# Kernel tuning notes

Hardware: AMD Instinct MI355X
Metric: run time of the kernel (lower is better)

Reference implementation:

```python
import jax, jax.numpy as jnp
import numpy as np

C = 16       # celltypes
N = 20000    # nodes per PPI graph
D = 192      # in_channels == out_channels*heads (residual constraint)
H = 3        # node_heads
CO = 64      # out_channels per head
E = 320000   # edges per PPI graph
T = 32       # tissue nodes
K = 8        # neighbors per tissue
M = C + T    # metagraph nodes
R = 4        # metagraph relations
EM = 256     # edges per metagraph relation
S = 128      # sem_att_channels
TU = 100     # tissue_update iterations


def setup_inputs():
    key = jax.random.key(0)
    k = jax.random.split(key, 16)
    g = lambda kk, shp, sc: jax.random.normal(kk, shp, jnp.float32) * sc
    return {
        "ppi_x": g(k[0], (C, N, D), 1.0),
        "metagraph_x": g(k[1], (M, D), 1.0),
        "ppi_lin": g(k[2], (C, D, H * CO), 0.07),
        "ppi_att_src": g(k[3], (C, H, CO), 0.1),
        "ppi_att_dst": g(k[4], (C, H, CO), 0.1),
        "ppi_bias": jnp.zeros((C, H * CO), jnp.float32),
        "meta_lin": g(k[5], (R, H * CO, H * CO), 0.07),
        "meta_att_src": g(k[6], (R, H, CO), 0.1),
        "meta_att_dst": g(k[7], (R, H, CO), 0.1),
        "meta_bias": jnp.zeros((R, H * CO), jnp.float32),
        "W_sem": g(k[8], (H * CO, S), 0.08),
        "b_sem": jnp.zeros((S,), jnp.float32),
        "q_sem": g(k[9], (S,), 0.1),
        "ppi_edges": jax.random.randint(k[10], (C, 2, E), 0, N, dtype=jnp.int32),
        "meta_edges": jax.random.randint(k[11], (R, 2, EM), 0, M, dtype=jnp.int32),
        "tissue_nb": jax.random.randint(k[12], (T, K), 0, M, dtype=jnp.int32),
    }


def gat(x, lin, att_s, att_d, bias, edge, n):
    """PyG-style GATConv, concat heads. x:[n,Din], edge:[2,E] (src,dst)."""
    h = (x @ lin).reshape(n, H, CO)
    a_s = (h * att_s).sum(-1)   # [n,H]
    a_d = (h * att_d).sum(-1)
    src, dst = edge[0], edge[1]
    e = jax.nn.leaky_relu(a_s[src] + a_d[dst], negative_slope=0.2)  # [E,H]
    emax = jax.lax.stop_gradient(jax.ops.segment_max(e, dst, num_segments=n))
    emax = jnp.where(jnp.isfinite(emax), emax, 0.0)
    ex = jnp.exp(e - emax[dst])
    denom = jax.ops.segment_sum(ex, dst, num_segments=n)          # [n,H]
    out = jax.ops.segment_sum(ex[:, :, None] * h[src], dst, num_segments=n)
    out = out / jnp.where(denom > 0.0, denom, 1.0)[:, :, None]
    return out.reshape(n, H * CO) + bias


def sem_attention(out, W, b, q):
    """Semantic attention over relations. out:[M,R,Dh]."""
    w = jnp.tanh(jnp.einsum('mrd,ds->mrs', out, W) + b)
    beta = jax.nn.softmax(jnp.einsum('mrs,s->mr', w, q), axis=1)
    return jnp.einsum('mrd,mr->md', out, beta)


def forward(ppi_x, metagraph_x, ppi_lin, ppi_att_src, ppi_att_dst, ppi_bias,
            meta_lin, meta_att_src, meta_att_dst, meta_bias,
            W_sem, b_sem, q_sem, ppi_edges, meta_edges, tissue_nb):
    mx = metagraph_x
    # residual GAT per celltype, mean-pooled into the metagraph celltype row
    for c in range(C):
        att = ppi_x[c] + gat(ppi_x[c], ppi_lin[c], ppi_att_src[c], ppi_att_dst[c],
                             ppi_bias[c], ppi_edges[c], N)
        mx = mx.at[c].add(att.mean(0))
    # sequential (Gauss-Seidel) tissue-neighbor mean diffusion, TU sweeps
    def step(m, t):
        return m.at[C + t].set(m[tissue_nb[t]].mean(0)), None
    def sweep(m, _):
        m, _ = jax.lax.scan(step, m, jnp.arange(T))
        return m, None
    mx, _ = jax.lax.scan(sweep, mx, None, length=TU)
    # multi-relation metagraph GAT + semantic attention fusion
    outs = jnp.stack([gat(mx, meta_lin[r], meta_att_src[r], meta_att_dst[r],
                          meta_bias[r], meta_edges[r], M) for r in range(R)], axis=1)
    outs = jax.nn.relu(outs)  # torch applies relu after stacking
    return sem_attention(outs, W_sem, b_sem, q_sem)


def reference(ppi_x, metagraph_x, ppi_lin, ppi_att_src, ppi_att_dst, ppi_bias,
              meta_lin, meta_att_src, meta_att_dst, meta_bias,
              W_sem, b_sem, q_sem, ppi_edges, meta_edges, tissue_nb):
    return forward(ppi_x, metagraph_x, ppi_lin, ppi_att_src, ppi_att_dst, ppi_bias,
                   meta_lin, meta_att_src, meta_att_dst, meta_bias,
                   W_sem, b_sem, q_sem, ppi_edges, meta_edges, tissue_nb)
```

## Files before the change

### kernel.cpp

```cpp
#include <hip/hip_runtime.h>

#define CT 16
#define NN 20000
#define EE 320000
#define MM 48
#define RR 4
#define EMM 256
#define NRANGE 64
#define NPR 313
#define CAP 5632
#define MAGIC 13721941ULL

#define OFF_MEANX 0
#define OFF_P     3072
#define OFF_CNTD  12288
#define OFF_CNTS  13312
#define ZERO_FLOATS 14336
#define OFF_COMB  14336
#define OFF_AS    2574336
#define OFF_AD    3854336
#define OFF_U     5134336
#define OFF_V     5143552
#define OFF_MX    5152768
#define OFF_HH    5161984
#define OFF_OUTS  5198848
#define OFF_BIND  5235712
#define OFF_BINS  11002880

__device__ inline unsigned bucket_of(int d) {
    return (unsigned)(((unsigned long long)(unsigned)d * MAGIC) >> 32);
}

__global__ __launch_bounds__(192) void k_prep(const float* __restrict__ lin,
        const float* __restrict__ as_g, const float* __restrict__ ad_g,
        float* __restrict__ U, float* __restrict__ V) {
    int c = blockIdx.x, d = threadIdx.x;
    const float* L  = lin + ((size_t)c * 192 + d) * 192;
    const float* As = as_g + c * 192;
    const float* Ad = ad_g + c * 192;
#pragma unroll
    for (int h = 0; h < 3; ++h) {
        float u = 0.f, v = 0.f;
        for (int j = 0; j < 64; ++j) {
            float lv = L[h * 64 + j];
            u += lv * As[h * 64 + j];
            v += lv * Ad[h * 64 + j];
        }
        U[c * 576 + h * 192 + d] = u;
        V[c * 576 + h * 192 + d] = v;
    }
}

__global__ __launch_bounds__(256) void k_front(const int* __restrict__ edges,
        int* __restrict__ cntD, int* __restrict__ cntS,
        int* __restrict__ binD, int* __restrict__ binS,
        const float* __restrict__ x, const float* __restrict__ U,
        const float* __restrict__ V, float* __restrict__ a_s,
        float* __restrict__ a_d, float* __restrict__ meanx) {
    __shared__ __align__(16) float smem[3456];
    int tid = threadIdx.x;
    if (blockIdx.x < 1024) {
        int wg = blockIdx.x;
        int ct = (wg & 7) * 2 + ((wg >> 3) & 1);
        int part = wg >> 4;
        int wave = tid >> 6;
        int* histD = (int*)smem;
        int* histS = histD + 256;
        int* curD  = histS + 256;
        int* curS  = curD + 64;
        if (tid < NRANGE) {
            histD[0 * 64 + tid] = 0; histD[1 * 64 + tid] = 0;
            histD[2 * 64 + tid] = 0; histD[3 * 64 + tid] = 0;
            histS[0 * 64 + tid] = 0; histS[1 * 64 + tid] = 0;
            histS[2 * 64 + tid] = 0; histS[3 * 64 + tid] = 0;
        }
        __syncthreads();
        const int* srcp = edges + (size_t)ct * 2 * EE;
        const int* dstp = srcp + EE;
        const int4* s4 = (const int4*)srcp;
        const int4* d4 = (const int4*)dstp;
        int base4 = part * 1250;
        for (int i = tid; i < 1250; i += 256) {
            int4 dv = d4[base4 + i];
            int4 sv = s4[base4 + i];
            atomicAdd(&histD[wave * 64 + bucket_of(dv.x)], 1);
            atomicAdd(&histD[wave * 64 + bucket_of(dv.y)], 1);
            atomicAdd(&histD[wave * 64 + bucket_of(dv.z)], 1);
            atomicAdd(&histD[wave * 64 + bucket_of(dv.w)], 1);
            atomicAdd(&histS[wave * 64 + bucket_of(sv.x)], 1);
            atomicAdd(&histS[wave * 64 + bucket_of(sv.y)], 1);
            atomicAdd(&histS[wave * 64 + bucket_of(sv.z)], 1);
            atomicAdd(&histS[wave * 64 + bucket_of(sv.w)], 1);
        }
        __syncthreads();
        if (tid < NRANGE) {
            int t = histD[tid] + histD[64 + tid] + histD[128 + tid] + histD[192 + tid];
            curD[tid] = atomicAdd(&cntD[ct * NRANGE + tid], t);
            int t2 = histS[tid] + histS[64 + tid] + histS[128 + tid] + histS[192 + tid];
            curS[tid] = atomicAdd(&cntS[ct * NRANGE + tid], t2);
        }
        __syncthreads();
        int* bD = binD + (size_t)ct * NRANGE * CAP;
        int* bS = binS + (size_t)ct * NRANGE * CAP;
#define EMIT2(ss, dd) { int pk = ((ss) << 15) | (dd); \
        unsigned bd = bucket_of(dd); int so = atomicAdd(&curD[bd], 1); \
        if (so < CAP) bD[bd * CAP + so] = pk; \
        unsigned bs = bucket_of(ss); int s2 = atomicAdd(&curS[bs], 1); \
        if (s2 < CAP) bS[bs * CAP + s2] = pk; }
        for (int i = tid; i < 1250; i += 256) {
            int4 dv = d4[base4 + i];
            int4 sv = s4[base4 + i];
            EMIT2(sv.x, dv.x); EMIT2(sv.y, dv.y); EMIT2(sv.z, dv.z); EMIT2(sv.w, dv.w);
        }
#undef EMIT2
    } else {
        int idx = blockIdx.x - 1024;
        int c = idx & 15;
        int start = (idx >> 4) * 160;
        int lane = tid & 63;
        int wave = tid >> 6;
        float* A = smem;
        float* blk = smem + 3264;
        if (tid < 192) blk[tid] = 0.f;
        float u0[3], u1[3], u2[3], v0[3], v1[3], v2[3];
#pragma unroll
        for (int h = 0; h < 3; ++h) {
            u0[h] = U[c * 576 + h * 192 + lane];
            u1[h] = U[c * 576 + h * 192 + 64 + lane];
            u2[h] = U[c * 576 + h * 192 + 128 + lane];
            v0[h] = V[c * 576 + h * 192 + lane];
            v1[h] = V[c * 576 + h * 192 + 64 + lane];
            v2[h] = V[c * 576 + h * 192 + 128 + lane];
        }
        __syncthreads();
        const float* xc = x + (size_t)c * NN * 192;
        float* asn = a_s + (size_t)c * NN * 4;
        float* adn = a_d + (size_t)c * NN * 4;
        float m0 = 0.f, m1 = 0.f, m2 = 0.f;
        float* Aa = A + (wave * 2) * 408;
        float* Ab = A + (wave * 2 + 1) * 408;
        int rrow = lane >> 3, seg = lane & 7;
        for (int i = 0; i < 20; ++i) {
            int na = start + wave + 8 * i;
            int nb = na + 4;
            const float* xa = xc + (size_t)na * 192;
            const float* xb = xc + (size_t)nb * 192;
            float xa0 = xa[lane], xa1 = xa[64 + lane], xa2 = xa[128 + lane];
            float xb0 = xb[lane], xb1 = xb[64 + lane], xb2 = xb[128 + lane];
            m0 += xa0 + xb0; m1 += xa1 + xb1; m2 += xa2 + xb2;
            Aa[0 * 68 + lane] = xa0 * u0[0] + xa1 * u1[0] + xa2 * u2[0];
            Aa[1 * 68 + lane] = xa0 * u0[1] + xa1 * u1[1] + xa2 * u2[1];
            Aa[2 * 68 + lane] = xa0 * u0[2] + xa1 * u1[2] + xa2 * u2[2];
            Aa[3 * 68 + lane] = xa0 * v0[0] + xa1 * v1[0] + xa2 * v2[0];
            Aa[4 * 68 + lane] = xa0 * v0[1] + xa1 * v1[1] + xa2 * v2[1];
            Aa[5 * 68 + lane] = xa0 * v0[2] + xa1 * v1[2] + xa2 * v2[2];
            Ab[0 * 68 + lane] = xb0 * u0[0] + xb1 * u1[0] + xb2 * u2[0];
            Ab[1 * 68 + lane] = xb0 * u0[1] + xb1 * u1[1] + xb2 * u2[1];
            Ab[2 * 68 + lane] = xb0 * u0[2] + xb1 * u1[2] + xb2 * u2[2];
            Ab[3 * 68 + lane] = xb0 * v0[0] + xb1 * v1[0] + xb2 * v2[0];
            Ab[4 * 68 + lane] = xb0 * v0[1] + xb1 * v1[1] + xb2 * v2[1];
            Ab[5 * 68 + lane] = xb0 * v0[2] + xb1 * v1[2] + xb2 * v2[2];
            float sa = 0.f, sb = 0.f;
            if (lane < 48) {
                const float4* pa = (const float4*)(Aa + rrow * 68 + seg * 8);
                const float4* pb = (const float4*)(Ab + rrow * 68 + seg * 8);
                float4 a0 = pa[0], a1 = pa[1];
                float4 b0 = pb[0], b1 = pb[1];
                sa = ((a0.x + a0.y) + (a0.z + a0.w)) + ((a1.x + a1.y) + (a1.z + a1.w));
                sb = ((b0.x + b0.y) + (b0.z + b0.w)) + ((b1.x + b1.y) + (b1.z + b1.w));
            }
            sa += __shfl_xor(sa, 1, 64); sb += __shfl_xor(sb, 1, 64);
            sa += __shfl_xor(sa, 2, 64); sb += __shfl_xor(sb, 2, 64);
            sa += __shfl_xor(sa, 4, 64); sb += __shfl_xor(sb, 4, 64);
            if (lane < 48 && seg == 0) {
                if (rrow < 3) { asn[na * 4 + rrow] = sa;     asn[nb * 4 + rrow] = sb; }
                else          { adn[na * 4 + rrow - 3] = sa; adn[nb * 4 + rrow - 3] = sb; }
            }
        }
        atomicAdd(&blk[lane], m0);
        atomicAdd(&blk[64 + lane], m1);
        atomicAdd(&blk[128 + lane], m2);
        __syncthreads();
        if (tid < 192) atomicAdd(&meanx[c * 192 + tid], blk[tid]);
    }
}

__device__ inline void map_ct(int wg, int& ct, int& j) {
    int xcd = wg & 7;
    ct = xcd * 2 + ((wg >> 3) & 1);
    j = wg >> 4;
}

__global__ __launch_bounds__(512) void k_eden_b(const int* __restrict__ bin,
        const int* __restrict__ cnt, const float* __restrict__ a_s,
        const float* __restrict__ a_d, float* __restrict__ comb) {
    int ct, bkt;
    map_ct(blockIdx.x, ct, bkt);
    int lo = bkt * NPR;
    int nnode = NN - lo < NPR ? NN - lo : NPR;
    int tid = threadIdx.x;
    __shared__ float adl[NPR * 3];
    __shared__ float den[NPR * 3];
    const float4* as4 = (const float4*)(a_s + (size_t)ct * NN * 4);
    const float4* ad4 = (const float4*)(a_d + (size_t)ct * NN * 4);
    for (int m = tid; m < nnode; m += 512) {
        float4 v = ad4[lo + m];
        adl[m * 3] = v.x; adl[m * 3 + 1] = v.y; adl[m * 3 + 2] = v.z;
    }
    for (int o = tid; o < nnode * 3; o += 512) den[o] = 0.f;
    __syncthreads();
    int n = cnt[ct * NRANGE + bkt]; if (n > CAP) n = CAP;
    const int* bc = bin + ((size_t)ct * NRANGE + bkt) * CAP;
    for (int i = tid; i < n; i += 512) {
        int v = bc[i];
        int d = v & 32767, s = v >> 15;
        int dl = d - lo;
        float4 av = as4[s];
        float e0 = av.x + adl[dl * 3];     e0 = e0 >= 0.f ? e0 : 0.2f * e0;
        float e1 = av.y + adl[dl * 3 + 1]; e1 = e1 >= 0.f ? e1 : 0.2f * e1;
        float e2 = av.z + adl[dl * 3 + 2]; e2 = e2 >= 0.f ? e2 : 0.2f * e2;
        atomicAdd(&den[dl * 3],     __expf(e0));
        atomicAdd(&den[dl * 3 + 1], __expf(e1));
        atomicAdd(&den[dl * 3 + 2], __expf(e2));
    }
    __syncthreads();
    float4* cb = (float4*)(comb + (size_t)ct * NN * 8);
    for (int m = tid; m < nnode; m += 512) {
        float d0 = den[m * 3], d1 = den[m * 3 + 1], d2 = den[m * 3 + 2];
        float4 a, b;
        a.x = adl[m * 3]; a.y = adl[m * 3 + 1]; a.z = adl[m * 3 + 2]; a.w = 0.f;
        b.x = d0 > 0.f ? 1.f / d0 : 0.f;
        b.y = d1 > 0.f ? 1.f / d1 : 0.f;
        b.z = d2 > 0.f ? 1.f / d2 : 0.f;
        b.w = 0.f;
        cb[(size_t)(lo + m) * 2]     = a;
        cb[(size_t)(lo + m) * 2 + 1] = b;
    }
}

__global__ __launch_bounds__(512) void k_es_p(const int* __restrict__ bin,
        const int* __restrict__ cnt, const float* __restrict__ a_s,
        const float* __restrict__ comb, const float* __restrict__ x,
        float* __restrict__ p) {
    int ct, bkt;
    map_ct(blockIdx.x, ct, bkt);
    int lo = bkt * NPR;
    int nnode = NN - lo < NPR ? NN - lo : NPR;
    int tid = threadIdx.x;
    __shared__ float asl[NPR * 3];
    __shared__ float sl[NPR * 3];
    __shared__ float blk[576];
    const float4* as4 = (const float4*)(a_s + (size_t)ct * NN * 4);
    const float4* cb  = (const float4*)(comb + (size_t)ct * NN * 8);
    for (int m = tid; m < nnode; m += 512) {
        float4 v = as4[lo + m];
        asl[m * 3] = v.x; asl[m * 3 + 1] = v.y; asl[m * 3 + 2] = v.z;
    }
    for (int o = tid; o < nnode * 3; o += 512) sl[o] = 0.f;
    for (int o = tid; o < 576; o += 512) blk[o] = 0.f;
    __syncthreads();
    int n = cnt[ct * NRANGE + bkt]; if (n > CAP) n = CAP;
    const int* bc = bin + ((size_t)ct * NRANGE + bkt) * CAP;
    for (int i = tid; i < n; i += 512) {
        int v = bc[i];
        int d = v & 32767, s = v >> 15;
        int slc = s - lo;
        float4 av = cb[(size_t)d * 2];
        float4 dv = cb[(size_t)d * 2 + 1];
        float e0 = asl[slc * 3]     + av.x; e0 = e0 >= 0.f ? e0 : 0.2f * e0;
        float e1 = asl[slc * 3 + 1] + av.y; e1 = e1 >= 0.f ? e1 : 0.2f * e1;
        float e2 = asl[slc * 3 + 2] + av.z; e2 = e2 >= 0.f ? e2 : 0.2f * e2;
        atomicAdd(&sl[slc * 3],     __expf(e0) * dv.x);
        atomicAdd(&sl[slc * 3 + 1], __expf(e1) * dv.y);
        atomicAdd(&sl[slc * 3 + 2], __expf(e2) * dv.z);
    }
    __syncthreads();
    int lane = tid & 63;
    int wave = tid >> 6;
    const float* xc = x + (size_t)ct * NN * 192;
    float a00 = 0, a01 = 0, a02 = 0, a10 = 0, a11 = 0, a12 = 0, a20 = 0, a21 = 0, a22 = 0;
    for (int m = wave; m < nnode; m += 8) {
        float s0 = sl[m * 3], s1 = sl[m * 3 + 1], s2 = sl[m * 3 + 2];
        const float* xr = xc + (size_t)(lo + m) * 192;
        float x0 = xr[lane], x1 = xr[64 + lane], x2 = xr[128 + lane];
        a00 += s0 * x0; a01 += s0 * x1; a02 += s0 * x2;
        a10 += s1 * x0; a11 += s1 * x1; a12 += s1 * x2;
        a20 += s2 * x0; a21 += s2 * x1; a22 += s2 * x2;
    }
    atomicAdd(&blk[0 * 192 + lane], a00);
    atomicAdd(&blk[0 * 192 + 64 + lane], a01);
    atomicAdd(&blk[0 * 192 + 128 + lane], a02);
    atomicAdd(&blk[1 * 192 + lane], a10);
    atomicAdd(&blk[1 * 192 + 64 + lane], a11);
    atomicAdd(&blk[1 * 192 + 128 + lane], a12);
    atomicAdd(&blk[2 * 192 + lane], a20);
    atomicAdd(&blk[2 * 192 + 64 + lane], a21);
    atomicAdd(&blk[2 * 192 + 128 + lane], a22);
    __syncthreads();
    for (int o = tid; o < 576; o += 512) atomicAdd(&p[ct * 576 + o], blk[o]);
}

__global__ __launch_bounds__(192) void k_mx(const float* __restrict__ mgx,
        const float* __restrict__ meanx, const float* __restrict__ p,
        const float* __restrict__ lin, const float* __restrict__ bias,
        float* __restrict__ mx) {
    int m = blockIdx.x, j = threadIdx.x;
    if (m < CT) {
        int h = j >> 6;
        const float* ph = p + m * 576 + h * 192;
        const float* L = lin + (size_t)m * 36864;
        float acc = 0.f;
        for (int k = 0; k < 192; ++k) acc += ph[k] * L[k * 192 + j];
        mx[m * 192 + j] = mgx[m * 192 + j] + (meanx[m * 192 + j] + acc) * (1.f / NN)
                          + bias[m * 192 + j];
    } else {
        mx[m * 192 + j] = mgx[m * 192 + j];
    }
}

__global__ __launch_bounds__(256) void k_tissue(const int* __restrict__ nb,
        float* __restrict__ mx) {
    __shared__ float B[3][2304];
    int tid = threadIdx.x;
    for (int o = tid; o < 2304; o += 256) {
        float idv = ((o / 48) == (o % 48)) ? 1.f : 0.f;
        B[0][o] = idv;
        B[1][o] = idv;
    }
    __syncthreads();
    if (tid < 48) {
        int j = tid;
        for (int t = 0; t < 32; ++t) {
            float acc = 0.f;
#pragma unroll
            for (int k = 0; k < 8; ++k) {
                int idx = nb[t * 8 + k];
                acc += B[0][idx * 48 + j];
            }
            B[0][(16 + t) * 48 + j] = acc * 0.125f;
        }
    }
    __syncthreads();
    int iP = 0, iR = 1, iT = 2;
    int e = 100;
    while (e) {
        if (e & 1) {
            for (int o = tid; o < 2304; o += 256) {
                int rr = o / 48, cc = o - rr * 48;
                float acc = 0.f;
                for (int k = 0; k < 48; ++k) acc += B[iR][rr * 48 + k] * B[iP][k * 48 + cc];
                B[iT][o] = acc;
            }
            __syncthreads();
            int t_ = iR; iR = iT; iT = t_;
        }
        e >>= 1;
        if (e) {
            for (int o = tid; o < 2304; o += 256) {
                int rr = o / 48, cc = o - rr * 48;
                float acc = 0.f;
                for (int k = 0; k < 48; ++k) acc += B[iP][rr * 48 + k] * B[iP][k * 48 + cc];
                B[iT][o] = acc;
            }
            __syncthreads();
            int t_ = iP; iP = iT; iT = t_;
        }
    }
    float accv[24];
#pragma unroll
    for (int i = 0; i < 24; ++i) {
        int o = tid + i * 256;
        int rr = o / 192, d = o - rr * 192;
        float acc = 0.f;
        for (int k = 0; k < 48; ++k) acc += B[iR][(16 + rr) * 48 + k] * mx[k * 192 + d];
        accv[i] = acc;
    }
    __syncthreads();
#pragma unroll
    for (int i = 0; i < 24; ++i) {
        int o = tid + i * 256;
        int rr = o / 192, d = o - rr * 192;
        mx[(16 + rr) * 192 + d] = accv[i];
    }
}

__global__ __launch_bounds__(192) void k_meta_h(const float* __restrict__ mx,
        const float* __restrict__ lin, float* __restrict__ hh) {
    int r = blockIdx.x, m = blockIdx.y, j = threadIdx.x;
    const float* L = lin + (size_t)r * 36864;
    const float* xr = mx + m * 192;
    float acc = 0.f;
    for (int k = 0; k < 192; ++k) acc += xr[k] * L[k * 192 + j];
    hh[((size_t)r * 48 + m) * 192 + j] = acc;
}

__global__ __launch_bounds__(256) void k_meta_edge(const float* __restrict__ hh,
        const float* __restrict__ att_s, const float* __restrict__ att_d,
        const float* __restrict__ bias, const int* __restrict__ edges,
        float* __restrict__ outs) {
    int r = blockIdx.x;
    int tid = threadIdx.x;
    __shared__ float as_[48][3], ad_[48][3], den[48][3];
    const float* hr = hh + (size_t)r * 48 * 192;
    float* og = outs + (size_t)r * 48 * 192;
    if (tid < 144) {
        int m = tid / 3, h = tid % 3;
        const float* As = att_s + r * 192 + h * 64;
        const float* Ad = att_d + r * 192 + h * 64;
        float s_ = 0.f, d_ = 0.f;
        for (int j = 0; j < 64; ++j) {
            float hv = hr[m * 192 + h * 64 + j];
            s_ += hv * As[j]; d_ += hv * Ad[j];
        }
        as_[m][h] = s_; ad_[m][h] = d_;
        den[m][h] = 0.f;
    }
    for (int o = tid; o < 9216; o += 256) og[o] = bias[r * 192 + (o % 192)];
    __syncthreads();
    int s = edges[(size_t)r * 2 * EMM + tid];
    int d = edges[(size_t)r * 2 * EMM + EMM + tid];
    float e0 = as_[s][0] + ad_[d][0]; e0 = e0 >= 0.f ? e0 : 0.2f * e0;
    float e1 = as_[s][1] + ad_[d][1]; e1 = e1 >= 0.f ? e1 : 0.2f * e1;
    float e2 = as_[s][2] + ad_[d][2]; e2 = e2 >= 0.f ? e2 : 0.2f * e2;
    float ex0 = __expf(e0), ex1 = __expf(e1), ex2 = __expf(e2);
    atomicAdd(&den[d][0], ex0);
    atomicAdd(&den[d][1], ex1);
    atomicAdd(&den[d][2], ex2);
    __syncthreads();
    float w0 = ex0 / den[d][0], w1 = ex1 / den[d][1], w2 = ex2 / den[d][2];
    const float* hs = hr + s * 192;
    float* od = og + d * 192;
    for (int j = 0; j < 64; ++j)        atomicAdd(&od[j], w0 * hs[j]);
    for (int j = 64; j < 128; ++j)      atomicAdd(&od[j], w1 * hs[j]);
    for (int j = 128; j < 192; ++j)     atomicAdd(&od[j], w2 * hs[j]);
}

__global__ __launch_bounds__(128) void k_sem(const float* __restrict__ outs,
        const float* __restrict__ W, const float* __restrict__ b,
        const float* __restrict__ q, float* __restrict__ out) {
    int m = blockIdx.x, s = threadIdx.x;
    __shared__ float ro[4][192];
    __shared__ float red[4][128];
    __shared__ float beta[4];
    for (int o = s; o < 768; o += 128) {
        int r = o / 192, d = o - r * 192;
        float v = outs[((size_t)r * 48 + m) * 192 + d];
        ro[r][d] = v > 0.f ? v : 0.f;
    }
    __syncthreads();
    float p0 = 0, p1 = 0, p2 = 0, p3 = 0;
    for (int d = 0; d < 192; ++d) {
        float wv = W[d * 128 + s];
        p0 += ro[0][d] * wv; p1 += ro[1][d] * wv; p2 += ro[2][d] * wv; p3 += ro[3][d] * wv;
    }
    float bb = b[s], qq = q[s];
    red[0][s] = tanhf(p0 + bb) * qq;
    red[1][s] = tanhf(p1 + bb) * qq;
    red[2][s] = tanhf(p2 + bb) * qq;
    red[3][s] = tanhf(p3 + bb) * qq;
    __syncthreads();
    for (int off = 64; off >= 1; off >>= 1) {
        if (s < off) {
            red[0][s] += red[0][s + off];
            red[1][s] += red[1][s + off];
            red[2][s] += red[2][s + off];
            red[3][s] += red[3][s + off];
        }
        __syncthreads();
    }
    if (s == 0) {
        float s0 = red[0][0], s1 = red[1][0], s2 = red[2][0], s3 = red[3][0];
        float mx4 = fmaxf(fmaxf(s0, s1), fmaxf(s2, s3));
        float e0 = __expf(s0 - mx4), e1 = __expf(s1 - mx4);
        float e2 = __expf(s2 - mx4), e3 = __expf(s3 - mx4);
        float inv = 1.f / (e0 + e1 + e2 + e3);
        beta[0] = e0 * inv; beta[1] = e1 * inv; beta[2] = e2 * inv; beta[3] = e3 * inv;
    }
    __syncthreads();
    for (int d = s; d < 192; d += 128) {
        float acc = ro[0][d] * beta[0] + ro[1][d] * beta[1]
                  + ro[2][d] * beta[2] + ro[3][d] * beta[3];
        out[m * 192 + d] = acc;
    }
}

extern "C" void kernel_launch(void* const* d_in, const int* in_sizes, int n_in,
                              void* d_out, int out_size, void* d_ws, size_t ws_size,
                              hipStream_t stream) {
    const float* ppi_x    = (const float*)d_in[0];
    const float* mgx      = (const float*)d_in[1];
    const float* ppi_lin  = (const float*)d_in[2];
    const float* ppi_as   = (const float*)d_in[3];
    const float* ppi_ad   = (const float*)d_in[4];
    const float* ppi_b    = (const float*)d_in[5];
    const float* meta_lin = (const float*)d_in[6];
    const float* meta_as  = (const float*)d_in[7];
    const float* meta_ad  = (const float*)d_in[8];
    const float* meta_b   = (const float*)d_in[9];
    const float* W_sem    = (const float*)d_in[10];
    const float* b_sem    = (const float*)d_in[11];
    const float* q_sem    = (const float*)d_in[12];
    const int*   ppi_e    = (const int*)d_in[13];
    const int*   meta_e   = (const int*)d_in[14];
    const int*   tnb      = (const int*)d_in[15];

    float* ws   = (float*)d_ws;
    float* mnx  = ws + OFF_MEANX;
    float* pac  = ws + OFF_P;
    int*   cntD = (int*)(ws + OFF_CNTD);
    int*   cntS = (int*)(ws + OFF_CNTS);
    float* comb = ws + OFF_COMB;
    float* a_s  = ws + OFF_AS;
    float* a_d  = ws + OFF_AD;
    float* U    = ws + OFF_U;
    float* V    = ws + OFF_V;
    float* mx   = ws + OFF_MX;
    float* hh   = ws + OFF_HH;
    float* outs = ws + OFF_OUTS;
    int*   binD = (int*)(ws + OFF_BIND);
    int*   binS = (int*)(ws + OFF_BINS);

    hipMemsetAsync(d_ws, 0, (size_t)ZERO_FLOATS * sizeof(float), stream);
    k_prep<<<16, 192, 0, stream>>>(ppi_lin, ppi_as, ppi_ad, U, V);
    k_front<<<3024, 256, 0, stream>>>(ppi_e, cntD, cntS, binD, binS,
                                      ppi_x, U, V, a_s, a_d, mnx);
    k_eden_b<<<1024, 512, 0, stream>>>(binD, cntD, a_s, a_d, comb);
    k_es_p<<<1024, 512, 0, stream>>>(binS, cntS, a_s, comb, ppi_x, pac);
    k_mx<<<48, 192, 0, stream>>>(mgx, mnx, pac, ppi_lin, ppi_b, mx);
    k_tissue<<<1, 256, 0, stream>>>(tnb, mx);
    k_meta_h<<<dim3(4, 48), 192, 0, stream>>>(mx, meta_lin, hh);
    k_meta_edge<<<4, 256, 0, stream>>>(hh, meta_as, meta_ad, meta_b, meta_e, outs);
    k_sem<<<48, 128, 0, stream>>>(outs, W_sem, b_sem, q_sem, (float*)d_out);
}
```

Before: 556.8 us.

## Overlap tissue matrix-power computation with edge pass and vectorize x accumulation

The single-block kernel that builds the 48x48 tissue diffusion operator and raises it to the 100th power now runs as an extra block of the large edge-scatter kernel. It no longer depends on mx, so it overlaps with the bulk work instead of running serially. A small 48-block kernel then applies the resulting matrix to mx. The per-node x accumulation in the edge kernel also switches to float4 loads using 48 lanes. This adds a launch and an intermediate buffer, and the extra block could become the tail of the edge kernel if it runs longer than the other blocks.

```diff
diff --git a/kernel.cpp b/kernel.cpp
--- a/kernel.cpp
+++ b/kernel.cpp
@@ -26,6 +26,8 @@
 #define OFF_OUTS  5198848
 #define OFF_BIND  5235712
 #define OFF_BINS  11002880
+#define OFF_W     16770048
+#define OFF_MX2   16772352
 
 __device__ inline unsigned bucket_of(int d) {
     return (unsigned)(((unsigned long long)(unsigned)d * MAGIC) >> 32);
@@ -241,15 +243,69 @@
 __global__ __launch_bounds__(512) void k_es_p(const int* __restrict__ bin,
         const int* __restrict__ cnt, const float* __restrict__ a_s,
         const float* __restrict__ comb, const float* __restrict__ x,
-        float* __restrict__ p) {
+        float* __restrict__ p, const int* __restrict__ nb,
+        float* __restrict__ Wout) {
+    __shared__ __align__(16) float smem[6912];
+    int tid = threadIdx.x;
+    if (blockIdx.x == 1024) {
+        float* B0 = smem;
+        float* B1 = smem + 2304;
+        float* B2 = smem + 4608;
+        float* B[3] = {B0, B1, B2};
+        for (int o = tid; o < 2304; o += 512) {
+            float idv = ((o / 48) == (o % 48)) ? 1.f : 0.f;
+            B0[o] = idv;
+            B1[o] = idv;
+        }
+        __syncthreads();
+        if (tid < 48) {
+            int j = tid;
+            for (int t = 0; t < 32; ++t) {
+                float acc = 0.f;
+#pragma unroll
+                for (int k = 0; k < 8; ++k) {
+                    int idx = nb[t * 8 + k];
+                    acc += B0[idx * 48 + j];
+                }
+                B0[(16 + t) * 48 + j] = acc * 0.125f;
+            }
+        }
+        __syncthreads();
+        int iP = 0, iR = 1, iT = 2;
+        int e = 100;
+        while (e) {
+            if (e & 1) {
+                for (int o = tid; o < 2304; o += 512) {
+                    int rr = o / 48, cc = o - rr * 48;
+                    float acc = 0.f;
+                    for (int k = 0; k < 48; ++k) acc += B[iR][rr * 48 + k] * B[iP][k * 48 + cc];
+                    B[iT][o] = acc;
+                }
+                __syncthreads();
+                int t_ = iR; iR = iT; iT = t_;
+            }
+            e >>= 1;
+            if (e) {
+                for (int o = tid; o < 2304; o += 512) {
+                    int rr = o / 48, cc = o - rr * 48;
+                    float acc = 0.f;
+                    for (int k = 0; k < 48; ++k) acc += B[iP][rr * 48 + k] * B[iP][k * 48 + cc];
+                    B[iT][o] = acc;
+                }
+                __syncthreads();
+                int t_ = iP; iP = iT; iT = t_;
+            }
+        }
+        for (int o = tid; o < 2304; o += 512) Wout[o] = B[iR][o];
+        return;
+    }
     int ct, bkt;
     map_ct(blockIdx.x, ct, bkt);
     int lo = bkt * NPR;
     int nnode = NN - lo < NPR ? NN - lo : NPR;
-    int tid = threadIdx.x;
-    __shared__ float asl[NPR * 3];
-    __shared__ float sl[NPR * 3];
-    __shared__ float blk[576];
+    float* asl = smem;
+    float* sl  = smem + 960;
+    float* blk = smem + 1920;
     const float4* as4 = (const float4*)(a_s + (size_t)ct * NN * 4);
     const float4* cb  = (const float4*)(comb + (size_t)ct * NN * 8);
     for (int m = tid; m < nnode; m += 512) {
@@ -277,25 +333,31 @@
     __syncthreads();
     int lane = tid & 63;
     int wave = tid >> 6;
-    const float* xc = x + (size_t)ct * NN * 192;
-    float a00 = 0, a01 = 0, a02 = 0, a10 = 0, a11 = 0, a12 = 0, a20 = 0, a21 = 0, a22 = 0;
-    for (int m = wave; m < nnode; m += 8) {
-        float s0 = sl[m * 3], s1 = sl[m * 3 + 1], s2 = sl[m * 3 + 2];
-        const float* xr = xc + (size_t)(lo + m) * 192;
-        float x0 = xr[lane], x1 = xr[64 + lane], x2 = xr[128 + lane];
-        a00 += s0 * x0; a01 += s0 * x1; a02 += s0 * x2;
-        a10 += s1 * x0; a11 += s1 * x1; a12 += s1 * x2;
-        a20 += s2 * x0; a21 += s2 * x1; a22 += s2 * x2;
-    }
-    atomicAdd(&blk[0 * 192 + lane], a00);
-    atomicAdd(&blk[0 * 192 + 64 + lane], a01);
-    atomicAdd(&blk[0 * 192 + 128 + lane], a02);
-    atomicAdd(&blk[1 * 192 + lane], a10);
-    atomicAdd(&blk[1 * 192 + 64 + lane], a11);
-    atomicAdd(&blk[1 * 192 + 128 + lane], a12);
-    atomicAdd(&blk[2 * 192 + lane], a20);
-    atomicAdd(&blk[2 * 192 + 64 + lane], a21);
-    atomicAdd(&blk[2 * 192 + 128 + lane], a22);
+    const float4* x4 = (const float4*)(x + (size_t)ct * NN * 192);
+    float4 a0 = make_float4(0.f, 0.f, 0.f, 0.f);
+    float4 a1 = a0, a2 = a0;
+    if (lane < 48) {
+        for (int m = wave; m < nnode; m += 8) {
+            float4 xv = x4[(size_t)(lo + m) * 48 + lane];
+            float s0 = sl[m * 3], s1 = sl[m * 3 + 1], s2 = sl[m * 3 + 2];
+            a0.x += xv.x * s0; a0.y += xv.y * s0; a0.z += xv.z * s0; a0.w += xv.w * s0;
+            a1.x += xv.x * s1; a1.y += xv.y * s1; a1.z += xv.z * s1; a1.w += xv.w * s1;
+            a2.x += xv.x * s2; a2.y += xv.y * s2; a2.z += xv.z * s2; a2.w += xv.w * s2;
+        }
+        int base = lane * 4;
+        atomicAdd(&blk[base],           a0.x);
+        atomicAdd(&blk[base + 1],       a0.y);
+        atomicAdd(&blk[base + 2],       a0.z);
+        atomicAdd(&blk[base + 3],       a0.w);
+        atomicAdd(&blk[192 + base],     a1.x);
+        atomicAdd(&blk[192 + base + 1], a1.y);
+        atomicAdd(&blk[192 + base + 2], a1.z);
+        atomicAdd(&blk[192 + base + 3], a1.w);
+        atomicAdd(&blk[384 + base],     a2.x);
+        atomicAdd(&blk[384 + base + 1], a2.y);
+        atomicAdd(&blk[384 + base + 2], a2.z);
+        atomicAdd(&blk[384 + base + 3], a2.w);
+    }
     __syncthreads();
     for (int o = tid; o < 576; o += 512) atomicAdd(&p[ct * 576 + o], blk[o]);
 }
@@ -318,69 +380,15 @@
     }
 }
 
-__global__ __launch_bounds__(256) void k_tissue(const int* __restrict__ nb,
-        float* __restrict__ mx) {
-    __shared__ float B[3][2304];
-    int tid = threadIdx.x;
-    for (int o = tid; o < 2304; o += 256) {
-        float idv = ((o / 48) == (o % 48)) ? 1.f : 0.f;
-        B[0][o] = idv;
-        B[1][o] = idv;
-    }
-    __syncthreads();
-    if (tid < 48) {
-        int j = tid;
-        for (int t = 0; t < 32; ++t) {
-            float acc = 0.f;
-#pragma unroll
-            for (int k = 0; k < 8; ++k) {
-                int idx = nb[t * 8 + k];
-                acc += B[0][idx * 48 + j];
-            }
-            B[0][(16 + t) * 48 + j] = acc * 0.125f;
-        }
-    }
-    __syncthreads();
-    int iP = 0, iR = 1, iT = 2;
-    int e = 100;
-    while (e) {
-        if (e & 1) {
-            for (int o = tid; o < 2304; o += 256) {
-                int rr = o / 48, cc = o - rr * 48;
-                float acc = 0.f;
-                for (int k = 0; k < 48; ++k) acc += B[iR][rr * 48 + k] * B[iP][k * 48 + cc];
-                B[iT][o] = acc;
-            }
-            __syncthreads();
-            int t_ = iR; iR = iT; iT = t_;
-        }
-        e >>= 1;
-        if (e) {
-            for (int o = tid; o < 2304; o += 256) {
-                int rr = o / 48, cc = o - rr * 48;
-                float acc = 0.f;
-                for (int k = 0; k < 48; ++k) acc += B[iP][rr * 48 + k] * B[iP][k * 48 + cc];
-                B[iT][o] = acc;
-            }
-            __syncthreads();
-            int t_ = iP; iP = iT; iT = t_;
-        }
-    }
-    float accv[24];
-#pragma unroll
-    for (int i = 0; i < 24; ++i) {
-        int o = tid + i * 256;
-        int rr = o / 192, d = o - rr * 192;
+__global__ __launch_bounds__(192) void k_tapply(const float* __restrict__ W,
+        const float* __restrict__ mx, float* __restrict__ mx2) {
+    int m = blockIdx.x, j = threadIdx.x;
+    if (m < CT) {
+        mx2[m * 192 + j] = mx[m * 192 + j];
+    } else {
         float acc = 0.f;
-        for (int k = 0; k < 48; ++k) acc += B[iR][(16 + rr) * 48 + k] * mx[k * 192 + d];
-        accv[i] = acc;
-    }
-    __syncthreads();
-#pragma unroll
-    for (int i = 0; i < 24; ++i) {
-        int o = tid + i * 256;
-        int rr = o / 192, d = o - rr * 192;
-        mx[(16 + rr) * 192 + d] = accv[i];
+        for (int k = 0; k < 48; ++k) acc += W[m * 48 + k] * mx[k * 192 + j];
+        mx2[m * 192 + j] = acc;
     }
 }
 
@@ -519,16 +527,18 @@
     float* outs = ws + OFF_OUTS;
     int*   binD = (int*)(ws + OFF_BIND);
     int*   binS = (int*)(ws + OFF_BINS);
+    float* Wt   = ws + OFF_W;
+    float* mx2  = ws + OFF_MX2;
 
     hipMemsetAsync(d_ws, 0, (size_t)ZERO_FLOATS * sizeof(float), stream);
     k_prep<<<16, 192, 0, stream>>>(ppi_lin, ppi_as, ppi_ad, U, V);
     k_front<<<3024, 256, 0, stream>>>(ppi_e, cntD, cntS, binD, binS,
                                       ppi_x, U, V, a_s, a_d, mnx);
     k_eden_b<<<1024, 512, 0, stream>>>(binD, cntD, a_s, a_d, comb);
-    k_es_p<<<1024, 512, 0, stream>>>(binS, cntS, a_s, comb, ppi_x, pac);
+    k_es_p<<<1025, 512, 0, stream>>>(binS, cntS, a_s, comb, ppi_x, pac, tnb, Wt);
     k_mx<<<48, 192, 0, stream>>>(mgx, mnx, pac, ppi_lin, ppi_b, mx);
-    k_tissue<<<1, 256, 0, stream>>>(tnb, mx);
-    k_meta_h<<<dim3(4, 48), 192, 0, stream>>>(mx, meta_lin, hh);
+    k_tapply<<<48, 192, 0, stream>>>(Wt, mx, mx2);
+    k_meta_h<<<dim3(4, 48), 192, 0, stream>>>(mx2, meta_lin, hh);
     k_meta_edge<<<4, 256, 0, stream>>>(hh, meta_as, meta_ad, meta_b, meta_e, outs);
     k_sem<<<48, 128, 0, stream>>>(outs, W_sem, b_sem, q_sem, (float*)d_out);
 }
```

Measured after the change: 533.7 us. 4.1% less time.
